# Performance work log

Measured on AMD Instinct MI355X. Metric: run time of the kernel, lower is better.

Reference implementation:

```python
import jax, jax.numpy as jnp
import numpy as np

SEQ = 4096
STATE_DIM = 512
ACTION_DIM = 496
T_DIM = 16
EMBED = STATE_DIM + ACTION_DIM + T_DIM  # 1024
HEADS = 4
HEAD_DIM = EMBED // HEADS
FF = 4096
N_EXP = 8
TOP_K = 2
EPS = 1e-5


def _ln(x, g, b):
    m = jnp.mean(x, -1, keepdims=True)
    v = jnp.var(x, -1, keepdims=True)
    return (x - m) * jax.lax.rsqrt(v + EPS) * g + b


def setup_inputs() -> dict:
    key = jax.random.key(0)
    ks = jax.random.split(key, 24)
    s = lambda k, shape, scale=0.02: jax.random.normal(k, shape, dtype=jnp.float32) * scale
    return {
        "x": jax.random.normal(ks[0], (SEQ, ACTION_DIM), dtype=jnp.float32),
        "time": jax.random.randint(ks[1], (SEQ,), 0, 6),
        "state": jax.random.normal(ks[2], (SEQ, 1, STATE_DIM), dtype=jnp.float32),
        "time_table": s(ks[3], (6, T_DIM), 1.0),
        "expert_w": s(ks[4], (N_EXP, EMBED, EMBED)),   # [n, in, out]
        "expert_b": jnp.zeros((N_EXP, EMBED), jnp.float32),
        "gate_w": s(ks[5], (EMBED, N_EXP)),
        "gate_b": jnp.zeros((N_EXP,), jnp.float32),
        "in_proj_w": s(ks[6], (EMBED, 3 * EMBED)),
        "in_proj_b": jnp.zeros((3 * EMBED,), jnp.float32),
        "out_proj_w": s(ks[7], (EMBED, EMBED)),
        "out_proj_b": jnp.zeros((EMBED,), jnp.float32),
        "ln1_g": jnp.ones((EMBED,), jnp.float32),
        "ln1_b": jnp.zeros((EMBED,), jnp.float32),
        "ff1_w": s(ks[8], (EMBED, FF)),
        "ff1_b": jnp.zeros((FF,), jnp.float32),
        "ff2_w": s(ks[9], (FF, ACTION_DIM)),
        "ff2_b": jnp.zeros((ACTION_DIM,), jnp.float32),
        "ln2_g": jnp.ones((ACTION_DIM,), jnp.float32),
        "ln2_b": jnp.zeros((ACTION_DIM,), jnp.float32),
    }


def reference(x, time, state, time_table, expert_w, expert_b, gate_w, gate_b,
              in_proj_w, in_proj_b, out_proj_w, out_proj_b,
              ln1_g, ln1_b, ff1_w, ff1_b, ff2_w, ff2_b, ln2_g, ln2_b):
    # combine inputs -> [S, EMBED]
    t_emb = time_table[time]                      # [S, t_dim]
    h = jnp.concatenate([x, t_emb, state[:, 0, :]], axis=-1)

    # MoE: softmax gate, top-k combine over densely-computed expert outputs
    gate = jax.nn.softmax(h @ gate_w + gate_b, axis=-1)      # [S, N]
    scores, idx = jax.lax.top_k(gate, TOP_K)                 # [S, K]
    all_out = jnp.einsum('se,nef->snf', h, expert_w) + expert_b[None]  # [S, N, E]
    comb = jnp.zeros_like(gate).at[jnp.arange(SEQ)[:, None], idx].add(scores)
    moe = jnp.einsum('sn,snf->sf', comb, all_out)            # [S, E]

    # multi-head self-attention (torch nn.MultiheadAttention, unbatched)
    qkv = moe @ in_proj_w + in_proj_b
    q, k, v = jnp.split(qkv, 3, axis=-1)
    q = q.reshape(SEQ, HEADS, HEAD_DIM) * (HEAD_DIM ** -0.5)
    k = k.reshape(SEQ, HEADS, HEAD_DIM)
    v = v.reshape(SEQ, HEADS, HEAD_DIM)
    att = jax.nn.softmax(jnp.einsum('shd,thd->hst', q, k), axis=-1)
    ao = jnp.einsum('hst,thd->shd', att, v).reshape(SEQ, EMBED)
    ao = ao @ out_proj_w + out_proj_b

    out1 = _ln(moe + ao, ln1_g, ln1_b)
    ff = jax.nn.relu(out1 @ ff1_w + ff1_b) @ ff2_w + ff2_b   # [S, action_dim]
    return _ln(ff, ln2_g, ln2_b)
```

## Files before the change

kernel.cpp:

```cpp
#include <hip/hip_runtime.h>
#include <hip/hip_bf16.h>
#include <hip/hip_fp8.h>

typedef __hip_bfloat16 hb;
typedef __bf16 bf16x8 __attribute__((ext_vector_type(8)));
typedef float f32x4 __attribute__((ext_vector_type(4)));

#define SEQ 4096
#define EMBED 1024
#define NHEAD 4
#define HDIM 256
#define FFD 4096
#define NEXP 8
#define ADIM 496
#define NSLOT 9216

static __device__ __forceinline__ float b2f(hb x) { return __bfloat162float(x); }
static __device__ __forceinline__ hb f2b(float x) { return __float2bfloat16(x); }
static __device__ __forceinline__ unsigned char f2e4m3(float v) {
  __hip_fp8_e4m3 t(v);
  return t.__x;
}
static __device__ __forceinline__ unsigned char f2e4m3_fast(float x) {
  unsigned u = __float_as_uint(x);
  u += 0x7FFFFu + ((u >> 20) & 1u);
  return (unsigned char)((u >> 20) - 960u);
}

#define GLOAD_LDS16(g, l)                                                      \
  __builtin_amdgcn_global_load_lds(                                            \
      (const __attribute__((address_space(1))) void*)(g),                      \
      (__attribute__((address_space(3))) void*)(l), 16, 0, 0)

#define GEMM_KLOOP64(KMAX)                                                     \
  for (int kt = 0; kt < (KMAX); kt += 64) {                                    \
    GLOAD_LDS16(Ag + kt, sA + wave * 512);                                     \
    GLOAD_LDS16(Ag + kt + 32, sA + 4096 + wave * 512);                         \
    GLOAD_LDS16(Ag + kt + 64 * lda_, sA + 2048 + wave * 512);                  \
    GLOAD_LDS16(Ag + kt + 64 * lda_ + 32, sA + 6144 + wave * 512);             \
    GLOAD_LDS16(Bg + kt, sB + wave * 512);                                     \
    GLOAD_LDS16(Bg + kt + 32, sB + 4096 + wave * 512);                         \
    GLOAD_LDS16(Bg + kt + 64 * ldb_, sB + 2048 + wave * 512);                  \
    GLOAD_LDS16(Bg + kt + 64 * ldb_ + 32, sB + 6144 + wave * 512);             \
    __syncthreads();                                                           \
    _Pragma("unroll") for (int ks = 0; ks < 2; ks++) {                         \
      bf16x8 av[4], bv[4];                                                     \
      _Pragma("unroll") for (int i = 0; i < 4; i++) {                          \
        const int row = wr * 64 + i * 16 + lm;                                 \
        av[i] = *(const bf16x8*)&sA[ks * 4096 + row * 32 + sw8];               \
      }                                                                        \
      _Pragma("unroll") for (int i = 0; i < 4; i++) {                          \
        const int row = wc * 64 + i * 16 + lm;                                 \
        bv[i] = *(const bf16x8*)&sB[ks * 4096 + row * 32 + sw8];               \
      }                                                                        \
      _Pragma("unroll") for (int i = 0; i < 4; i++)                            \
          _Pragma("unroll") for (int j = 0; j < 4; j++) acc[i][j] =            \
          __builtin_amdgcn_mfma_f32_16x16x32_bf16(av[i], bv[j], acc[i][j], 0,  \
                                                  0, 0);                       \
    }                                                                          \
    __syncthreads();                                                           \
  }

#define GEMM_PROLOGUE                                                          \
  const int m0 = blockIdx.y * 128, n0 = blockIdx.x * 128;                      \
  const int tid = threadIdx.x;                                                 \
  const int wave = tid >> 6, lane = tid & 63;                                  \
  const int quad = lane >> 4, lm = lane & 15;                                  \
  const int wr = wave >> 1, wc = wave & 1;                                     \
  const int r0 = tid >> 2;                                                     \
  const int cg = 8 * ((tid & 3) ^ ((tid >> 2) & 3));                           \
  const int sw8 = (quad ^ (lm & 3)) * 8;

#define EPILOGUE_B16(DST, LDC)                                                 \
  {                                                                            \
    hb* eb = smem + wave * 1024;                                               \
    _Pragma("unroll") for (int i = 0; i < 4; i++) {                            \
      _Pragma("unroll") for (int j = 0; j < 4; j++) {                          \
        const int c = ((j ^ quad) << 4) + lm;                                  \
        _Pragma("unroll") for (int rr = 0; rr < 4; rr++)                       \
            eb[(quad * 4 + rr) * 64 + c] = f2b(acc[i][j][rr]);                 \
      }                                                                        \
      _Pragma("unroll") for (int p = 0; p < 2; p++) {                          \
        const int r = p * 8 + (lane >> 3);                                     \
        const int cgc = lane & 7;                                              \
        const int gs = (cgc >> 1) ^ (r >> 2);                                  \
        const bf16x8 val =                                                     \
            *(const bf16x8*)&eb[r * 64 + gs * 16 + (cgc & 1) * 8];             \
        const long grow = m0 + wr * 64 + i * 16 + r;                           \
        *(bf16x8*)&DST[grow * (LDC) + n0 + wc * 64 + cgc * 8] = val;           \
      }                                                                        \
    }                                                                          \
  }

__global__ __launch_bounds__(256) void gemm_bt(
    const hb* __restrict__ A, long lda, long bA,
    const hb* __restrict__ B, long ldb, long bB,
    hb* __restrict__ C, long ldc, long bC,
    int K, const float* __restrict__ bias, int relu) {
  __shared__ __align__(16) hb smem[2 * 128 * 64];
  hb* sA = smem;
  hb* sB = smem + 8192;
  const int z = blockIdx.z;
  A += (long)z * bA;
  B += (long)z * bB;
  C += (long)z * bC;
  GEMM_PROLOGUE
  const long lda_ = lda, ldb_ = ldb;
  const hb* Ag = A + (long)(m0 + r0) * lda + cg;
  const hb* Bg = B + (long)(n0 + r0) * ldb + cg;

  f32x4 acc[4][4] = {};
  GEMM_KLOOP64(K)

  hb* eb = smem + wave * 1024;
#pragma unroll
  for (int i = 0; i < 4; i++) {
#pragma unroll
    for (int j = 0; j < 4; j++) {
      const float bval = bias ? bias[n0 + wc * 64 + j * 16 + lm] : 0.f;
      const int c = ((j ^ quad) << 4) + lm;
#pragma unroll
      for (int rr = 0; rr < 4; rr++) {
        float v = acc[i][j][rr] + bval;
        if (relu) v = fmaxf(v, 0.f);
        eb[(quad * 4 + rr) * 64 + c] = f2b(v);
      }
    }
#pragma unroll
    for (int p = 0; p < 2; p++) {
      const int r = p * 8 + (lane >> 3);
      const int cgc = lane & 7;
      const int gs = (cgc >> 1) ^ (r >> 2);
      const bf16x8 val = *(const bf16x8*)&eb[r * 64 + gs * 16 + (cgc & 1) * 8];
      const long grow = m0 + wr * 64 + i * 16 + r;
      *(bf16x8*)&C[grow * ldc + n0 + wc * 64 + cgc * 8] = val;
    }
  }
}

__global__ __launch_bounds__(256) void gemm_bt_exp(
    const hb* __restrict__ A, long lda, long bA,
    const hb* __restrict__ B, long ldb, long bB,
    unsigned char* __restrict__ C, long ldc, long bC,
    int K, float scale, hb* __restrict__ rsP) {
  __shared__ __align__(16) hb smem[2 * 128 * 64];
  hb* sA = smem;
  hb* sB = smem + 8192;
  const int z = blockIdx.z;
  A += (long)z * bA;
  B += (long)z * bB;
  C += (long)z * bC;
  GEMM_PROLOGUE
  const long lda_ = lda, ldb_ = ldb;
  const hb* Ag = A + (long)(m0 + r0) * lda + cg;
  const hb* Bg = B + (long)(n0 + r0) * ldb + cg;

  f32x4 acc[4][4] = {};
  GEMM_KLOOP64(K)

  unsigned char* eb8 = (unsigned char*)smem + wave * 1024;
  float* rbuf = (float*)sB;
  float rs[4][4];
#pragma unroll
  for (int i = 0; i < 4; i++) {
    float r4[4] = {0.f, 0.f, 0.f, 0.f};
#pragma unroll
    for (int j = 0; j < 4; j++) {
      const int c = ((j ^ quad) << 4) + lm;
#pragma unroll
      for (int rr = 0; rr < 4; rr++) {
        const float e =
            fminf(fmaxf(__expf(acc[i][j][rr] * scale), 0.015625f), 448.f);
        r4[rr] += e;
        eb8[(quad * 4 + rr) * 64 + c] = f2e4m3_fast(e);
      }
    }
#pragma unroll
    for (int rr = 0; rr < 4; rr++) {
      r4[rr] += __shfl_xor(r4[rr], 1);
      r4[rr] += __shfl_xor(r4[rr], 2);
      r4[rr] += __shfl_xor(r4[rr], 4);
      r4[rr] += __shfl_xor(r4[rr], 8);
      rs[i][rr] = r4[rr];
    }
    {
      const int r = lane >> 2;
      const int cgc = lane & 3;
      const f32x4 val =
          *(const f32x4*)&eb8[r * 64 + ((cgc ^ (r >> 2)) << 4)];
      const long grow = m0 + wr * 64 + i * 16 + r;
      *(f32x4*)&C[grow * ldc + n0 + wc * 64 + cgc * 16] = val;
    }
  }
  if (lm == 0) {
#pragma unroll
    for (int i = 0; i < 4; i++)
#pragma unroll
      for (int rr = 0; rr < 4; rr++)
        rbuf[(wr * 2 + wc) * 64 + i * 16 + quad * 4 + rr] = rs[i][rr];
  }
  __syncthreads();
  if (tid < 128) {
    const int lwr = tid >> 6, r64 = tid & 63;
    const float d = rbuf[lwr * 128 + r64] + rbuf[lwr * 128 + 64 + r64];
    rsP[((long)blockIdx.x * gridDim.z + z) * SEQ + m0 + lwr * 64 + r64] =
        f2b(d);
  }
}

__global__ __launch_bounds__(256) void pv_f8_splitk(
    const unsigned char* __restrict__ S, const unsigned char* __restrict__ Vt,
    hb* __restrict__ Cp) {
  const int z = blockIdx.z;
  const int head = z >> 1, split = z & 1;
  const unsigned char* A = S + (long)head * SEQ * SEQ + split * 2048;
  const unsigned char* B = Vt + ((long)head << 20) + split * 2048;
  hb* Cb = Cp + (long)z * SEQ * 256;
  __shared__ __align__(16) unsigned char smem8[16384];
  hb* smem = (hb*)smem8;
  unsigned char* sA8 = smem8;
  unsigned char* sB8 = smem8 + 8192;
  const int m0 = blockIdx.y * 128, n0 = blockIdx.x * 128;
  const int tid = threadIdx.x;
  const int wave = tid >> 6, lane = tid & 63;
  const int quad = lane >> 4, lm = lane & 15;
  const int wr = wave >> 1, wc = wave & 1;
  const int r8 = tid >> 2;
  const int cg8 = 16 * ((tid & 3) ^ (r8 & 3));
  const unsigned char* Ag = A + (long)(m0 + r8) * 4096 + cg8;
  const unsigned char* Bg = B + (long)(n0 + r8) * 4096 + cg8;

  f32x4 acc[4][4] = {};
  for (int kt = 0; kt < 2048; kt += 64) {
    GLOAD_LDS16(Ag + kt, sA8 + wave * 1024);
    GLOAD_LDS16(Ag + kt + 64 * 4096, sA8 + 4096 + wave * 1024);
    GLOAD_LDS16(Bg + kt, sB8 + wave * 1024);
    GLOAD_LDS16(Bg + kt + 64 * 4096, sB8 + 4096 + wave * 1024);
    __syncthreads();
#pragma unroll
    for (int ks = 0; ks < 2; ks++) {
      long a8[4], b8[4];
#pragma unroll
      for (int i = 0; i < 4; i++) {
        const int row = wr * 64 + i * 16 + lm;
        a8[i] = *(const long*)&sA8[row * 64 +
                                   (((ks * 2 + (quad >> 1)) ^ (row & 3)) << 4) +
                                   (quad & 1) * 8];
      }
#pragma unroll
      for (int i = 0; i < 4; i++) {
        const int row = wc * 64 + i * 16 + lm;
        b8[i] = *(const long*)&sB8[row * 64 +
                                   (((ks * 2 + (quad >> 1)) ^ (row & 3)) << 4) +
                                   (quad & 1) * 8];
      }
#pragma unroll
      for (int i = 0; i < 4; i++)
#pragma unroll
        for (int j = 0; j < 4; j++)
          acc[i][j] = __builtin_amdgcn_mfma_f32_16x16x32_fp8_fp8(
              a8[i], b8[j], acc[i][j], 0, 0, 0);
    }
    __syncthreads();
  }
  EPILOGUE_B16(Cb, 256)
}

__global__ __launch_bounds__(256) void gemm_bt_splitk(
    const hb* __restrict__ A, long lda, long bA,
    const hb* __restrict__ B, long ldb, long bB,
    float* __restrict__ Cp, int ldcp, long pstride, int Ksub, int shift) {
  const int z = blockIdx.z;
  const int batch = z >> shift, split = z - (batch << shift);
  A += (long)batch * bA + (long)split * Ksub;
  B += (long)batch * bB + (long)split * Ksub;
  Cp += (long)z * pstride;
  __shared__ __align__(16) hb smem[2 * 128 * 64];
  hb* sA = smem;
  hb* sB = smem + 8192;
  GEMM_PROLOGUE
  const long lda_ = lda, ldb_ = ldb;
  const hb* Ag = A + (long)(m0 + r0) * lda + cg;
  const hb* Bg = B + (long)(n0 + r0) * ldb + cg;

  f32x4 acc[4][4] = {};
  GEMM_KLOOP64(Ksub)

  float* ef = (float*)smem + wave * 1024;
#pragma unroll
  for (int i = 0; i < 4; i++) {
#pragma unroll
    for (int j = 0; j < 4; j++) {
      const int c = ((j ^ quad) << 4) + lm;
#pragma unroll
      for (int rr = 0; rr < 4; rr++)
        ef[(quad * 4 + rr) * 64 + c] = acc[i][j][rr];
    }
#pragma unroll
    for (int p = 0; p < 4; p++) {
      const int r = p * 4 + (lane >> 4);
      const int cgc = lane & 15;
      const int gs = (cgc >> 2) ^ (r >> 2);
      const f32x4 val = *(const f32x4*)&ef[r * 64 + gs * 16 + (cgc & 3) * 4];
      const long grow = m0 + wr * 64 + i * 16 + r;
      *(f32x4*)&Cp[grow * ldcp + n0 + wc * 64 + cgc * 4] = val;
    }
  }
}

__global__ __launch_bounds__(256) void gemm_bt_splitk_b16(
    const hb* __restrict__ A, long lda, long bA,
    const hb* __restrict__ B, long ldb, long bB,
    hb* __restrict__ Cp, int ldcp, long pstride, int Ksub, int shift) {
  const int z = blockIdx.z;
  const int batch = z >> shift, split = z - (batch << shift);
  A += (long)batch * bA + (long)split * Ksub;
  B += (long)batch * bB + (long)split * Ksub;
  Cp += (long)z * pstride;
  __shared__ __align__(16) hb smem[2 * 128 * 64];
  hb* sA = smem;
  hb* sB = smem + 8192;
  GEMM_PROLOGUE
  const long lda_ = lda, ldb_ = ldb;
  const hb* Ag = A + (long)(m0 + r0) * lda + cg;
  const hb* Bg = B + (long)(n0 + r0) * ldb + cg;

  f32x4 acc[4][4] = {};
  GEMM_KLOOP64(Ksub)
  EPILOGUE_B16(Cp, ldcp)
}

__global__ __launch_bounds__(256) void reduce_splitk(
    const float* __restrict__ part, long pstride, int nsplit, int shift,
    hb* __restrict__ C, long ldc, long bC, int Nshift) {
  const long idx = (long)blockIdx.x * 256 + threadIdx.x;
  const int batch = blockIdx.y;
  float v = 0.f;
  for (int k = 0; k < nsplit; k++)
    v += part[(long)((batch << shift) + k) * pstride + idx];
  const long row = idx >> Nshift;
  const long col = idx & ((1 << Nshift) - 1);
  C[(long)batch * bC + row * ldc + col] = f2b(v);
}

__global__ __launch_bounds__(256) void reduce_pv(
    const hb* __restrict__ part, const hb* __restrict__ rsP,
    hb* __restrict__ ao) {
  const int row = blockIdx.x, head = blockIdx.y, tid = threadIdx.x;
  __shared__ float dsh;
  if (tid < 64) {
    float p = b2f(rsP[((long)(tid & 31) * NHEAD + head) * SEQ + row]);
#pragma unroll
    for (int o = 32; o; o >>= 1) p += __shfl_down(p, o);
    if (tid == 0) dsh = 0.5f * p;
  }
  __syncthreads();
  const float den = dsh;
  const long base = ((long)(head * 2) * SEQ + row) * 256 + tid;
  const float v = b2f(part[base]) + b2f(part[base + (long)SEQ * 256]);
  ao[(long)row * 1024 + head * 256 + tid] = f2b(v / den);
}

__global__ __launch_bounds__(256) void gemm_moe(
    const hb* __restrict__ h, const hb* __restrict__ expertT,
    const int* __restrict__ slot_token, const int* __restrict__ eblk,
    hb* __restrict__ slotout) {
  const int e = eblk[blockIdx.y];
  if (e < 0) return;
  __shared__ __align__(16) hb smem[2 * 128 * 64];
  hb* sA = smem;
  hb* sB = smem + 8192;
  GEMM_PROLOGUE
  const int t0 = slot_token[m0 + r0];
  const int t1 = slot_token[m0 + r0 + 64];
  const hb* B = expertT + ((long)e << 20);
  const hb* Ag0 = h + (long)t0 * EMBED + cg;
  const hb* Ag1 = h + (long)t1 * EMBED + cg;
  const hb* Bg = B + (long)(n0 + r0) * EMBED + cg;

  f32x4 acc[4][4] = {};
  for (int kt = 0; kt < EMBED; kt += 64) {
    GLOAD_LDS16(Ag0 + kt, sA + wave * 512);
    GLOAD_LDS16(Ag0 + kt + 32, sA + 4096 + wave * 512);
    GLOAD_LDS16(Ag1 + kt, sA + 2048 + wave * 512);
    GLOAD_LDS16(Ag1 + kt + 32, sA + 6144 + wave * 512);
    GLOAD_LDS16(Bg + kt, sB + wave * 512);
    GLOAD_LDS16(Bg + kt + 32, sB + 4096 + wave * 512);
    GLOAD_LDS16(Bg + kt + 64 * EMBED, sB + 2048 + wave * 512);
    GLOAD_LDS16(Bg + kt + 64 * EMBED + 32, sB + 6144 + wave * 512);
    __syncthreads();
#pragma unroll
    for (int ks = 0; ks < 2; ks++) {
      bf16x8 av[4], bv[4];
#pragma unroll
      for (int i = 0; i < 4; i++) {
        const int row = wr * 64 + i * 16 + lm;
        av[i] = *(const bf16x8*)&sA[ks * 4096 + row * 32 + sw8];
      }
#pragma unroll
      for (int i = 0; i < 4; i++) {
        const int row = wc * 64 + i * 16 + lm;
        bv[i] = *(const bf16x8*)&sB[ks * 4096 + row * 32 + sw8];
      }
#pragma unroll
      for (int i = 0; i < 4; i++)
#pragma unroll
        for (int j = 0; j < 4; j++)
          acc[i][j] = __builtin_amdgcn_mfma_f32_16x16x32_bf16(av[i], bv[j],
                                                              acc[i][j], 0, 0, 0);
    }
    __syncthreads();
  }
  EPILOGUE_B16(slotout, EMBED)
}

__global__ __launch_bounds__(256) void transpose_all(
    const float* __restrict__ expert_w, const float* __restrict__ in_proj_w,
    const float* __restrict__ out_proj_w, const float* __restrict__ ff1_w,
    const float* __restrict__ ff2_w, hb* __restrict__ expertT,
    hb* __restrict__ inprojT, hb* __restrict__ outprojT, hb* __restrict__ ff1T,
    hb* __restrict__ ff2T) {
  const int b = blockIdx.x;
  const float* in;
  hb* outp;
  int R, Cin, Cout, ldin, ldout, bx, by;
  if (b < 8192) {
    const int z = b >> 10, l = b & 1023;
    bx = l & 31; by = l >> 5;
    in = expert_w + (long)z * 1048576; outp = expertT + (long)z * 1048576;
    R = 1024; Cin = 1024; Cout = 1024; ldin = 1024; ldout = 1024;
  } else if (b < 11264) {
    const int l = b - 8192;
    bx = l % 96; by = l / 96;
    in = in_proj_w; outp = inprojT;
    R = 1024; Cin = 3072; Cout = 3072; ldin = 3072; ldout = 1024;
  } else if (b < 12288) {
    const int l = b - 11264;
    bx = l & 31; by = l >> 5;
    in = out_proj_w; outp = outprojT;
    R = 1024; Cin = 1024; Cout = 1024; ldin = 1024; ldout = 1024;
  } else if (b < 16384) {
    const int l = b - 12288;
    bx = l & 127; by = l >> 7;
    in = ff1_w; outp = ff1T;
    R = 1024; Cin = 4096; Cout = 4096; ldin = 4096; ldout = 1024;
  } else {
    const int l = b - 16384;
    bx = l & 15; by = l >> 4;
    in = ff2_w; outp = ff2T;
    R = 4096; Cin = 496; Cout = 512; ldin = 496; ldout = 4096;
  }
  __shared__ hb tile[32][33];
  const int c0 = bx * 32, r0 = by * 32;
  const int tx = threadIdx.x, ty = threadIdx.y;
#pragma unroll
  for (int i = 0; i < 32; i += 8) {
    const int r = r0 + ty + i, c = c0 + tx;
    hb v = f2b(0.f);
    if (r < R && c < Cin) v = f2b(in[(long)r * ldin + c]);
    tile[ty + i][tx] = v;
  }
  __syncthreads();
#pragma unroll
  for (int i = 0; i < 32; i += 8) {
    const int c = c0 + ty + i, r = r0 + tx;
    if (c < Cout && r < R) outp[(long)c * ldout + r] = tile[tx][ty + i];
  }
}

__global__ __launch_bounds__(256) void transpose_v(
    const hb* __restrict__ in, hb* __restrict__ out) {
  __shared__ hb tile[32][33];
  const int z = blockIdx.z;
  in += (long)z * 256;
  out += (long)z * 1048576;
  const int c0 = blockIdx.x * 32, r0 = blockIdx.y * 32;
  const int tx = threadIdx.x, ty = threadIdx.y;
#pragma unroll
  for (int i = 0; i < 32; i += 8)
    tile[ty + i][tx] = in[(long)(r0 + ty + i) * 3072 + c0 + tx];
  __syncthreads();
#pragma unroll
  for (int i = 0; i < 32; i += 8)
    out[(long)(c0 + ty + i) * 4096 + r0 + tx] = tile[tx][ty + i];
}

__global__ __launch_bounds__(256) void transpose_v8(
    const hb* __restrict__ in, unsigned char* __restrict__ out) {
  __shared__ hb tile[32][33];
  const int z = blockIdx.z;
  in += (long)z * 256;
  out += (long)z * 1048576;
  const int c0 = blockIdx.x * 32, r0 = blockIdx.y * 32;
  const int tx = threadIdx.x, ty = threadIdx.y;
#pragma unroll
  for (int i = 0; i < 32; i += 8)
    tile[ty + i][tx] = in[(long)(r0 + ty + i) * 3072 + c0 + tx];
  __syncthreads();
#pragma unroll
  for (int i = 0; i < 32; i += 8)
    out[(long)(c0 + ty + i) * 4096 + r0 + tx] = f2e4m3(b2f(tile[tx][ty + i]));
}

__global__ __launch_bounds__(256) void bh_gate_kernel(
    const float* __restrict__ x, const int* __restrict__ timev,
    const float* __restrict__ state, const float* __restrict__ ttab,
    const float* __restrict__ gw, const float* __restrict__ gb,
    hb* __restrict__ h, int* __restrict__ tok_e, float* __restrict__ tok_w) {
  const int s = blockIdx.x, tid = threadIdx.x;
  const int wv = tid >> 6, ln = tid & 63;
  const int t = timev[s];
  float acc[8] = {0, 0, 0, 0, 0, 0, 0, 0};
  for (int c = tid; c < EMBED; c += 256) {
    float v;
    if (c < ADIM)
      v = x[(long)s * ADIM + c];
    else if (c < ADIM + 16)
      v = ttab[t * 16 + (c - ADIM)];
    else
      v = state[(long)s * 512 + (c - 512)];
    h[(long)s * EMBED + c] = f2b(v);
    const float* g = gw + c * 8;
#pragma unroll
    for (int n = 0; n < 8; n++) acc[n] += v * g[n];
  }
#pragma unroll
  for (int o = 32; o; o >>= 1)
#pragma unroll
    for (int n = 0; n < 8; n++) acc[n] += __shfl_down(acc[n], o);
  __shared__ float red[4][8];
  if (ln == 0)
#pragma unroll
    for (int n = 0; n < 8; n++) red[wv][n] = acc[n];
  __syncthreads();
  if (tid == 0) {
    float lg[8], m = -1e30f;
    for (int n = 0; n < 8; n++) {
      lg[n] = red[0][n] + red[1][n] + red[2][n] + red[3][n] + gb[n];
      m = fmaxf(m, lg[n]);
    }
    float den = 0.f;
    for (int n = 0; n < 8; n++) {
      lg[n] = expf(lg[n] - m);
      den += lg[n];
    }
    for (int n = 0; n < 8; n++) lg[n] /= den;
    int i1 = 0;
    for (int n = 1; n < 8; n++)
      if (lg[n] > lg[i1]) i1 = n;
    int i2 = (i1 == 0) ? 1 : 0;
    for (int n = 0; n < 8; n++) {
      if (n == i1) continue;
      if (lg[n] > lg[i2]) i2 = n;
    }
    tok_e[2 * s] = i1;
    tok_w[2 * s] = lg[i1];
    tok_e[2 * s + 1] = i2;
    tok_w[2 * s + 1] = lg[i2];
  }
}

__global__ __launch_bounds__(256) void group_kernel(
    const int* __restrict__ tok_e, int* __restrict__ slot_token,
    int* __restrict__ token_slot, int* __restrict__ eblk) {
  __shared__ int cnt[8], off[9], cur[8];
  const int tid = threadIdx.x;
  if (tid < 8) cnt[tid] = 0;
  for (int i = tid; i < NSLOT; i += 256) slot_token[i] = 0;
  __syncthreads();
  for (int i = tid; i < 2 * SEQ; i += 256) atomicAdd(&cnt[tok_e[i]], 1);
  __syncthreads();
  if (tid == 0) {
    int o = 0;
    for (int n = 0; n < 8; n++) {
      off[n] = o;
      cur[n] = o;
      o += (cnt[n] + 127) & ~127;
    }
    off[8] = o;
  }
  __syncthreads();
  if (tid < NSLOT / 128) {
    const int rb = tid * 128;
    int e = -1;
    for (int n = 0; n < 8; n++)
      if (rb >= off[n] && rb < off[n + 1]) e = n;
    eblk[tid] = e;
  }
  for (int i = tid; i < 2 * SEQ; i += 256) {
    const int e = tok_e[i];
    const int slot = atomicAdd(&cur[e], 1);
    slot_token[slot] = i >> 1;
    token_slot[i] = slot;
  }
}

__global__ __launch_bounds__(256) void moe_combine_kernel(
    const hb* __restrict__ slotout, const int* __restrict__ token_slot,
    const float* __restrict__ tok_w, const int* __restrict__ tok_e,
    const float* __restrict__ eb, hb* __restrict__ moe) {
  const int s = blockIdx.x, tid = threadIdx.x;
  const int s0 = token_slot[2 * s], s1 = token_slot[2 * s + 1];
  const float w0 = tok_w[2 * s], w1 = tok_w[2 * s + 1];
  const int e0 = tok_e[2 * s], e1 = tok_e[2 * s + 1];
  const hb* r0 = slotout + (long)s0 * EMBED;
  const hb* r1 = slotout + (long)s1 * EMBED;
  const float* b0 = eb + e0 * EMBED;
  const float* b1 = eb + e1 * EMBED;
  for (int c = tid; c < EMBED; c += 256) {
    const float v = w0 * (b2f(r0[c]) + b0[c]) + w1 * (b2f(r1[c]) + b1[c]);
    moe[(long)s * EMBED + c] = f2b(v);
  }
}

__global__ __launch_bounds__(256) void softmax_fast(hb* __restrict__ S,
                                                    float scale) {
  const long row = blockIdx.x;
  const int tid = threadIdx.x, wv = tid >> 6, ln = tid & 63;
  hb* p = S + row * 4096 + tid * 16;
  __shared__ float red[4];
  bf16x8 a0 = *(const bf16x8*)p;
  bf16x8 a1 = *(const bf16x8*)(p + 8);
  float v[16];
#pragma unroll
  for (int i = 0; i < 8; i++) {
    v[i] = (float)a0[i];
    v[8 + i] = (float)a1[i];
  }
  float m = v[0];
#pragma unroll
  for (int i = 1; i < 16; i++) m = fmaxf(m, v[i]);
#pragma unroll
  for (int o = 32; o; o >>= 1) m = fmaxf(m, __shfl_down(m, o));
  if (ln == 0) red[wv] = m;
  __syncthreads();
  const float M = fmaxf(fmaxf(red[0], red[1]), fmaxf(red[2], red[3])) * scale;
  __syncthreads();
  float sum = 0.f;
#pragma unroll
  for (int i = 0; i < 16; i++) {
    v[i] = __expf(v[i] * scale - M);
    sum += v[i];
  }
#pragma unroll
  for (int o = 32; o; o >>= 1) sum += __shfl_down(sum, o);
  if (ln == 0) red[wv] = sum;
  __syncthreads();
  const float inv = 1.f / (red[0] + red[1] + red[2] + red[3]);
#pragma unroll
  for (int i = 0; i < 8; i++) {
    a0[i] = (__bf16)(v[i] * inv);
    a1[i] = (__bf16)(v[8 + i] * inv);
  }
  *(bf16x8*)p = a0;
  *(bf16x8*)(p + 8) = a1;
}

__global__ __launch_bounds__(256) void ln_kernel(
    const hb* __restrict__ in, long ldin, const hb* __restrict__ resid,
    long ldr, const float* __restrict__ g, const float* __restrict__ beta,
    hb* __restrict__ outb, long ldout, int ncol) {
  const int s = blockIdx.x, tid = threadIdx.x, wv = tid >> 6, ln = tid & 63;
  __shared__ float buf[1024];
  __shared__ float red[4];
  float sum = 0.f, sq = 0.f;
  for (int c = tid; c < ncol; c += 256) {
    float v = b2f(in[(long)s * ldin + c]);
    if (resid) v += b2f(resid[(long)s * ldr + c]);
    buf[c] = v;
    sum += v;
    sq += v * v;
  }
#pragma unroll
  for (int o = 32; o; o >>= 1) sum += __shfl_down(sum, o);
  if (ln == 0) red[wv] = sum;
  __syncthreads();
  const float S = red[0] + red[1] + red[2] + red[3];
  __syncthreads();
#pragma unroll
  for (int o = 32; o; o >>= 1) sq += __shfl_down(sq, o);
  if (ln == 0) red[wv] = sq;
  __syncthreads();
  const float Q = red[0] + red[1] + red[2] + red[3];
  const float mean = S / ncol;
  const float var = Q / ncol - mean * mean;
  const float r = rsqrtf(var + 1e-5f);
  for (int c = tid; c < ncol; c += 256)
    outb[(long)s * ldout + c] = f2b((buf[c] - mean) * r * g[c] + beta[c]);
}

__global__ __launch_bounds__(256) void ln2_red_kernel(
    const float* __restrict__ part, long pstride,
    const float* __restrict__ bias, const float* __restrict__ g,
    const float* __restrict__ beta, float* __restrict__ out) {
  const int s = blockIdx.x, tid = threadIdx.x, wv = tid >> 6, ln = tid & 63;
  __shared__ float buf[512];
  __shared__ float red[4];
  float sum = 0.f, sq = 0.f;
  for (int c = tid; c < ADIM; c += 256) {
    const long idx = (long)s * 512 + c;
    float v = part[idx] + part[pstride + idx] + part[2 * pstride + idx] +
              part[3 * pstride + idx] + bias[c];
    buf[c] = v;
    sum += v;
    sq += v * v;
  }
#pragma unroll
  for (int o = 32; o; o >>= 1) sum += __shfl_down(sum, o);
  if (ln == 0) red[wv] = sum;
  __syncthreads();
  const float S = red[0] + red[1] + red[2] + red[3];
  __syncthreads();
#pragma unroll
  for (int o = 32; o; o >>= 1) sq += __shfl_down(sq, o);
  if (ln == 0) red[wv] = sq;
  __syncthreads();
  const float Q = red[0] + red[1] + red[2] + red[3];
  const float mean = S / ADIM;
  const float var = Q / ADIM - mean * mean;
  const float r = rsqrtf(var + 1e-5f);
  for (int c = tid; c < ADIM; c += 256)
    out[(long)s * ADIM + c] = (buf[c] - mean) * r * g[c] + beta[c];
}

__global__ __launch_bounds__(256) void ln2_red_b16_kernel(
    const hb* __restrict__ part, long pstride,
    const float* __restrict__ bias, const float* __restrict__ g,
    const float* __restrict__ beta, float* __restrict__ out) {
  const int s = blockIdx.x, tid = threadIdx.x, wv = tid >> 6, ln = tid & 63;
  __shared__ float buf[512];
  __shared__ float red[4];
  float sum = 0.f, sq = 0.f;
  for (int c = tid; c < ADIM; c += 256) {
    const long idx = (long)s * 512 + c;
    float v = b2f(part[idx]) + b2f(part[pstride + idx]) +
              b2f(part[2 * pstride + idx]) + b2f(part[3 * pstride + idx]) +
              bias[c];
    buf[c] = v;
    sum += v;
    sq += v * v;
  }
#pragma unroll
  for (int o = 32; o; o >>= 1) sum += __shfl_down(sum, o);
  if (ln == 0) red[wv] = sum;
  __syncthreads();
  const float S = red[0] + red[1] + red[2] + red[3];
  __syncthreads();
#pragma unroll
  for (int o = 32; o; o >>= 1) sq += __shfl_down(sq, o);
  if (ln == 0) red[wv] = sq;
  __syncthreads();
  const float Q = red[0] + red[1] + red[2] + red[3];
  const float mean = S / ADIM;
  const float var = Q / ADIM - mean * mean;
  const float r = rsqrtf(var + 1e-5f);
  for (int c = tid; c < ADIM; c += 256)
    out[(long)s * ADIM + c] = (buf[c] - mean) * r * g[c] + beta[c];
}

extern "C" void kernel_launch(void* const* d_in, const int* in_sizes, int n_in,
                              void* d_out, int out_size, void* d_ws,
                              size_t ws_size, hipStream_t stream) {
  const float* x = (const float*)d_in[0];
  const int* timev = (const int*)d_in[1];
  const float* state = (const float*)d_in[2];
  const float* ttab = (const float*)d_in[3];
  const float* expert_w = (const float*)d_in[4];
  const float* expert_b = (const float*)d_in[5];
  const float* gate_w = (const float*)d_in[6];
  const float* gate_b = (const float*)d_in[7];
  const float* in_proj_w = (const float*)d_in[8];
  const float* in_proj_b = (const float*)d_in[9];
  const float* out_proj_w = (const float*)d_in[10];
  const float* out_proj_b = (const float*)d_in[11];
  const float* ln1_g = (const float*)d_in[12];
  const float* ln1_b = (const float*)d_in[13];
  const float* ff1_w = (const float*)d_in[14];
  const float* ff1_b = (const float*)d_in[15];
  const float* ff2_w = (const float*)d_in[16];
  const float* ff2_b = (const float*)d_in[17];
  const float* ln2_g = (const float*)d_in[18];
  const float* ln2_b = (const float*)d_in[19];
  float* out = (float*)d_out;

  char* w = (char*)d_ws;
  const long MB = 1048576;
  const bool big = ws_size >= (size_t)(192 * MB);

  hb* expertT = (hb*)(w + 0 * MB);
  hb* slotout = (hb*)(w + 16 * MB);
  hb* h = (hb*)(w + 35 * MB);
  hb* inprojT = (hb*)(w + 43 * MB);
  hb* outprojT = (hb*)(w + (big ? 168 : 49) * MB);
  hb* ff1T = (hb*)(w + (big ? 170 : 51) * MB);
  hb* ff2T = (hb*)(w + (big ? 178 : 59) * MB);
  const long metaOff = (big ? 190 : 63) * MB;
  int* tok_e = (int*)(w + metaOff);
  float* tok_w = (float*)(w + metaOff + 32768);
  int* slot_token = (int*)(w + metaOff + 65536);
  int* token_slot = (int*)(w + metaOff + 102400);
  int* eblk = (int*)(w + metaOff + 135168);
  hb* rsP = (hb*)(w + metaOff + 163840);
  hb* moe = (hb*)(w + (big ? 152 : 64) * MB);
  hb* qkv = (hb*)(w + (big ? 0 : 72) * MB);
  unsigned char* scores8 = (unsigned char*)(w + 24 * MB);
  hb* scores = (hb*)(w + 96 * MB);
  unsigned char* vt8 = (unsigned char*)(w + 160 * MB);
  hb* vt = (hb*)(w + 8 * MB);
  hb* ao = (hb*)(w + (big ? 182 : 0) * MB);
  hb* ao2 = (hb*)(w + (big ? 24 : 8) * MB);
  hb* out1 = (hb*)(w + (big ? 32 : 132) * MB);
  hb* ffmid = (hb*)(w + (big ? 40 : 96) * MB);
  float* part = (float*)(w + (big ? 72 : 16) * MB);
  hb* partb16 = (hb*)(w + (big ? 72 : 16) * MB);
  hb* pvpart = (hb*)(w + 0 * MB);
  (void)in_sizes; (void)n_in; (void)out_size;

  transpose_all<<<dim3(18432), dim3(32, 8), 0, stream>>>(
      expert_w, in_proj_w, out_proj_w, ff1_w, ff2_w, expertT, inprojT, outprojT,
      ff1T, ff2T);

  bh_gate_kernel<<<dim3(SEQ), 256, 0, stream>>>(x, timev, state, ttab, gate_w,
                                                gate_b, h, tok_e, tok_w);
  group_kernel<<<dim3(1), 256, 0, stream>>>(tok_e, slot_token, token_slot, eblk);

  gemm_moe<<<dim3(8, NSLOT / 128), 256, 0, stream>>>(h, expertT, slot_token,
                                                     eblk, slotout);
  moe_combine_kernel<<<dim3(SEQ), 256, 0, stream>>>(slotout, token_slot, tok_w,
                                                    tok_e, expert_b, moe);

  gemm_bt<<<dim3(24, 32, 1), 256, 0, stream>>>(moe, 1024, 0, inprojT, 1024, 0,
                                               qkv, 3072, 0, 1024, in_proj_b, 0);
  if (big)
    transpose_v8<<<dim3(8, 128, 4), dim3(32, 8), 0, stream>>>(qkv + 2048, vt8);
  else
    transpose_v<<<dim3(8, 128, 4), dim3(32, 8), 0, stream>>>(qkv + 2048, vt);

  if (big) {
    gemm_bt_exp<<<dim3(32, 32, 4), 256, 0, stream>>>(
        qkv, 3072, 256, qkv + 1024, 3072, 256, scores8, 4096, (long)SEQ * SEQ,
        HDIM, 0.0625f, rsP);
    pv_f8_splitk<<<dim3(2, 32, 8), 256, 0, stream>>>(scores8, vt8, pvpart);
    reduce_pv<<<dim3(4096, 4), 256, 0, stream>>>(pvpart, rsP, ao);
  } else {
    for (int hp = 0; hp < 2; ++hp) {
      const hb* qb = qkv + hp * 512;
      const hb* kb = qkv + 1024 + hp * 512;
      gemm_bt<<<dim3(32, 32, 2), 256, 0, stream>>>(
          qb, 3072, 256, kb, 3072, 256, scores, 4096, (long)SEQ * SEQ, HDIM,
          nullptr, 0);
      softmax_fast<<<dim3(2 * SEQ), 256, 0, stream>>>(scores, 0.0625f);
      gemm_bt_splitk<<<dim3(2, 32, 8), 256, 0, stream>>>(
          scores, 4096, (long)SEQ * SEQ, vt + (long)hp * 2097152, 4096,
          1048576L, part, 256, (long)SEQ * 256, 1024, 2);
      reduce_splitk<<<dim3(4096, 2), 256, 0, stream>>>(
          part, (long)SEQ * 256, 4, 2, ao + hp * 512, 1024, 256, 8);
    }
  }

  gemm_bt<<<dim3(8, 32, 1), 256, 0, stream>>>(ao, 1024, 0, outprojT, 1024, 0,
                                              ao2, 1024, 0, 1024, out_proj_b, 0);
  ln_kernel<<<dim3(SEQ), 256, 0, stream>>>(moe, 1024, ao2, 1024, ln1_g, ln1_b,
                                           out1, 1024, 1024);

  gemm_bt<<<dim3(32, 32, 1), 256, 0, stream>>>(out1, 1024, 0, ff1T, 1024, 0,
                                               ffmid, 4096, 0, 1024, ff1_b, 1);
  if (big) {
    gemm_bt_splitk_b16<<<dim3(4, 32, 4), 256, 0, stream>>>(
        ffmid, 4096, 0, ff2T, 4096, 0, partb16, 512, (long)SEQ * 512, 1024, 2);
    ln2_red_b16_kernel<<<dim3(SEQ), 256, 0, stream>>>(
        partb16, (long)SEQ * 512, ff2_b, ln2_g, ln2_b, out);
  } else {
    gemm_bt_splitk<<<dim3(4, 32, 4), 256, 0, stream>>>(
        ffmid, 4096, 0, ff2T, 4096, 0, part, 512, (long)SEQ * 512, 1024, 2);
    ln2_red_kernel<<<dim3(SEQ), 256, 0, stream>>>(part, (long)SEQ * 512, ff2_b,
                                                  ln2_g, ln2_b, out);
  }
}
```

Measured before the change: 522.1 us.

## Vectorize weight transpose and elementwise kernels with wide loads and stores

Rewrites the fp32-to-bf16 weight transpose to use 64-row tiles, float4 reads, a swizzled shared tile and 16-byte bf16 stores, which halves the block count. The gate/concat, MoE combine, LayerNorm and PV-reduce kernels move from per-element accesses to 4-wide vector loads and stores. reduce_pv now handles four rows per block, and the duplicate lane sum is dropped from its denominator. The aim is to cut memory-transaction overhead in these bandwidth-bound kernels. The cost is tighter alignment and divisibility assumptions on the data shapes.

```diff
diff --git a/kernel.cpp b/kernel.cpp
--- a/kernel.cpp
+++ b/kernel.cpp
@@ -4,6 +4,7 @@
 
 typedef __hip_bfloat16 hb;
 typedef __bf16 bf16x8 __attribute__((ext_vector_type(8)));
+typedef __bf16 bf16x4 __attribute__((ext_vector_type(4)));
 typedef float f32x4 __attribute__((ext_vector_type(4)));
 
 #define SEQ 4096
@@ -346,19 +347,26 @@
 __global__ __launch_bounds__(256) void reduce_pv(
     const hb* __restrict__ part, const hb* __restrict__ rsP,
     hb* __restrict__ ao) {
-  const int row = blockIdx.x, head = blockIdx.y, tid = threadIdx.x;
-  __shared__ float dsh;
-  if (tid < 64) {
-    float p = b2f(rsP[((long)(tid & 31) * NHEAD + head) * SEQ + row]);
-#pragma unroll
-    for (int o = 32; o; o >>= 1) p += __shfl_down(p, o);
-    if (tid == 0) dsh = 0.5f * p;
-  }
-  __syncthreads();
-  const float den = dsh;
-  const long base = ((long)(head * 2) * SEQ + row) * 256 + tid;
-  const float v = b2f(part[base]) + b2f(part[base + (long)SEQ * 256]);
-  ao[(long)row * 1024 + head * 256 + tid] = f2b(v / den);
+  const int rb = blockIdx.x * 4, head = blockIdx.y, tid = threadIdx.x;
+  __shared__ float dsh[4];
+  if (tid < 128) {
+    const int r = tid >> 5, nb = tid & 31;
+    float p = b2f(rsP[((long)nb * NHEAD + head) * SEQ + rb + r]);
+#pragma unroll
+    for (int o = 16; o; o >>= 1) p += __shfl_down(p, o, 32);
+    if (nb == 0) dsh[r] = p;
+  }
+  __syncthreads();
+  const int r = tid >> 6, c4 = (tid & 63) * 4;
+  const float den = dsh[r];
+  const long base = ((long)(head * 2) * SEQ + rb + r) * 256 + c4;
+  const bf16x4 p0 = *(const bf16x4*)&part[base];
+  const bf16x4 p1 = *(const bf16x4*)&part[base + (long)SEQ * 256];
+  bf16x4 o4;
+#pragma unroll
+  for (int k = 0; k < 4; k++)
+    o4[k] = (__bf16)(((float)p0[k] + (float)p1[k]) / den);
+  *(bf16x4*)&ao[(long)(rb + r) * 1024 + head * 256 + c4] = o4;
 }
 
 __global__ __launch_bounds__(256) void gemm_moe(
@@ -423,48 +431,57 @@
   const int b = blockIdx.x;
   const float* in;
   hb* outp;
-  int R, Cin, Cout, ldin, ldout, bx, by;
-  if (b < 8192) {
-    const int z = b >> 10, l = b & 1023;
+  int Cin, ldin, ldout, bx, by;
+  if (b < 4096) {
+    const int z = b >> 9, l = b & 511;
     bx = l & 31; by = l >> 5;
     in = expert_w + (long)z * 1048576; outp = expertT + (long)z * 1048576;
-    R = 1024; Cin = 1024; Cout = 1024; ldin = 1024; ldout = 1024;
-  } else if (b < 11264) {
-    const int l = b - 8192;
+    Cin = 1024; ldin = 1024; ldout = 1024;
+  } else if (b < 5632) {
+    const int l = b - 4096;
     bx = l % 96; by = l / 96;
     in = in_proj_w; outp = inprojT;
-    R = 1024; Cin = 3072; Cout = 3072; ldin = 3072; ldout = 1024;
-  } else if (b < 12288) {
-    const int l = b - 11264;
+    Cin = 3072; ldin = 3072; ldout = 1024;
+  } else if (b < 6144) {
+    const int l = b - 5632;
     bx = l & 31; by = l >> 5;
     in = out_proj_w; outp = outprojT;
-    R = 1024; Cin = 1024; Cout = 1024; ldin = 1024; ldout = 1024;
-  } else if (b < 16384) {
-    const int l = b - 12288;
+    Cin = 1024; ldin = 1024; ldout = 1024;
+  } else if (b < 8192) {
+    const int l = b - 6144;
     bx = l & 127; by = l >> 7;
     in = ff1_w; outp = ff1T;
-    R = 1024; Cin = 4096; Cout = 4096; ldin = 4096; ldout = 1024;
+    Cin = 4096; ldin = 4096; ldout = 1024;
   } else {
-    const int l = b - 16384;
+    const int l = b - 8192;
     bx = l & 15; by = l >> 4;
     in = ff2_w; outp = ff2T;
-    R = 4096; Cin = 496; Cout = 512; ldin = 496; ldout = 4096;
-  }
-  __shared__ hb tile[32][33];
-  const int c0 = bx * 32, r0 = by * 32;
-  const int tx = threadIdx.x, ty = threadIdx.y;
-#pragma unroll
-  for (int i = 0; i < 32; i += 8) {
-    const int r = r0 + ty + i, c = c0 + tx;
-    hb v = f2b(0.f);
-    if (r < R && c < Cin) v = f2b(in[(long)r * ldin + c]);
-    tile[ty + i][tx] = v;
-  }
-  __syncthreads();
-#pragma unroll
-  for (int i = 0; i < 32; i += 8) {
-    const int c = c0 + ty + i, r = r0 + tx;
-    if (c < Cout && r < R) outp[(long)c * ldout + r] = tile[tx][ty + i];
+    Cin = 496; ldin = 496; ldout = 4096;
+  }
+  __shared__ hb tile[32][72];
+  const int c0 = bx * 32, r0 = by * 64;
+  const int t = threadIdx.x;
+  {
+    const int rr = t >> 2, cb = (t & 3) * 8;
+    const int c = c0 + cb;
+    float v[8] = {0, 0, 0, 0, 0, 0, 0, 0};
+    if (c < Cin) {
+      const f32x4 p0 = *(const f32x4*)&in[(long)(r0 + rr) * ldin + c];
+      const f32x4 p1 = *(const f32x4*)&in[(long)(r0 + rr) * ldin + c + 4];
+#pragma unroll
+      for (int k = 0; k < 4; k++) { v[k] = p0[k]; v[4 + k] = p1[k]; }
+    }
+#pragma unroll
+    for (int j = 0; j < 8; j++) {
+      const int cidx = cb + j;
+      tile[cidx][rr ^ ((((cidx) >> 3) & 3) << 3)] = f2b(v[j]);
+    }
+  }
+  __syncthreads();
+  {
+    const int oc = t >> 3, seg = t & 7;
+    const bf16x8 val = *(const bf16x8*)&tile[oc][(seg ^ ((oc >> 3) & 3)) * 8];
+    *(bf16x8*)&outp[(long)(c0 + oc) * ldout + r0 + seg * 8] = val;
   }
 }
 
@@ -510,19 +527,24 @@
   const int s = blockIdx.x, tid = threadIdx.x;
   const int wv = tid >> 6, ln = tid & 63;
   const int t = timev[s];
+  const int c = tid * 4;
+  f32x4 v4;
+  if (c < ADIM)
+    v4 = *(const f32x4*)&x[(long)s * ADIM + c];
+  else if (c < 512)
+    v4 = *(const f32x4*)&ttab[t * 16 + (c - ADIM)];
+  else
+    v4 = *(const f32x4*)&state[(long)s * 512 + (c - 512)];
+  bf16x4 h4;
+#pragma unroll
+  for (int k = 0; k < 4; k++) h4[k] = (__bf16)v4[k];
+  *(bf16x4*)&h[(long)s * EMBED + c] = h4;
   float acc[8] = {0, 0, 0, 0, 0, 0, 0, 0};
-  for (int c = tid; c < EMBED; c += 256) {
-    float v;
-    if (c < ADIM)
-      v = x[(long)s * ADIM + c];
-    else if (c < ADIM + 16)
-      v = ttab[t * 16 + (c - ADIM)];
-    else
-      v = state[(long)s * 512 + (c - 512)];
-    h[(long)s * EMBED + c] = f2b(v);
-    const float* g = gw + c * 8;
-#pragma unroll
-    for (int n = 0; n < 8; n++) acc[n] += v * g[n];
+#pragma unroll
+  for (int k = 0; k < 4; k++) {
+    const float* g = gw + (c + k) * 8;
+#pragma unroll
+    for (int n = 0; n < 8; n++) acc[n] += v4[k] * g[n];
   }
 #pragma unroll
   for (int o = 32; o; o >>= 1)
@@ -603,14 +625,16 @@
   const int s0 = token_slot[2 * s], s1 = token_slot[2 * s + 1];
   const float w0 = tok_w[2 * s], w1 = tok_w[2 * s + 1];
   const int e0 = tok_e[2 * s], e1 = tok_e[2 * s + 1];
-  const hb* r0 = slotout + (long)s0 * EMBED;
-  const hb* r1 = slotout + (long)s1 * EMBED;
-  const float* b0 = eb + e0 * EMBED;
-  const float* b1 = eb + e1 * EMBED;
-  for (int c = tid; c < EMBED; c += 256) {
-    const float v = w0 * (b2f(r0[c]) + b0[c]) + w1 * (b2f(r1[c]) + b1[c]);
-    moe[(long)s * EMBED + c] = f2b(v);
-  }
+  const int c = tid * 4;
+  const bf16x4 a0 = *(const bf16x4*)&slotout[(long)s0 * EMBED + c];
+  const bf16x4 a1 = *(const bf16x4*)&slotout[(long)s1 * EMBED + c];
+  const f32x4 b0 = *(const f32x4*)&eb[e0 * EMBED + c];
+  const f32x4 b1 = *(const f32x4*)&eb[e1 * EMBED + c];
+  bf16x4 o4;
+#pragma unroll
+  for (int k = 0; k < 4; k++)
+    o4[k] = (__bf16)(w0 * ((float)a0[k] + b0[k]) + w1 * ((float)a1[k] + b1[k]));
+  *(bf16x4*)&moe[(long)s * EMBED + c] = o4;
 }
 
 __global__ __launch_bounds__(256) void softmax_fast(hb* __restrict__ S,
@@ -664,12 +688,24 @@
   __shared__ float buf[1024];
   __shared__ float red[4];
   float sum = 0.f, sq = 0.f;
-  for (int c = tid; c < ncol; c += 256) {
-    float v = b2f(in[(long)s * ldin + c]);
-    if (resid) v += b2f(resid[(long)s * ldr + c]);
-    buf[c] = v;
-    sum += v;
-    sq += v * v;
+  for (int c = tid * 4; c < ncol; c += 1024) {
+    const bf16x4 iv = *(const bf16x4*)&in[(long)s * ldin + c];
+#pragma unroll
+    for (int k = 0; k < 4; k++) {
+      float v = (float)iv[k];
+      buf[c + k] = v;
+    }
+    if (resid) {
+      const bf16x4 rv = *(const bf16x4*)&resid[(long)s * ldr + c];
+#pragma unroll
+      for (int k = 0; k < 4; k++) buf[c + k] += (float)rv[k];
+    }
+#pragma unroll
+    for (int k = 0; k < 4; k++) {
+      const float v = buf[c + k];
+      sum += v;
+      sq += v * v;
+    }
   }
 #pragma unroll
   for (int o = 32; o; o >>= 1) sum += __shfl_down(sum, o);
@@ -685,8 +721,15 @@
   const float mean = S / ncol;
   const float var = Q / ncol - mean * mean;
   const float r = rsqrtf(var + 1e-5f);
-  for (int c = tid; c < ncol; c += 256)
-    outb[(long)s * ldout + c] = f2b((buf[c] - mean) * r * g[c] + beta[c]);
+  for (int c = tid * 4; c < ncol; c += 1024) {
+    const f32x4 gv = *(const f32x4*)&g[c];
+    const f32x4 bv = *(const f32x4*)&beta[c];
+    bf16x4 o4;
+#pragma unroll
+    for (int k = 0; k < 4; k++)
+      o4[k] = (__bf16)((buf[c + k] - mean) * r * gv[k] + bv[k]);
+    *(bf16x4*)&outb[(long)s * ldout + c] = o4;
+  }
 }
 
 __global__ __launch_bounds__(256) void ln2_red_kernel(
@@ -731,14 +774,22 @@
   __shared__ float buf[512];
   __shared__ float red[4];
   float sum = 0.f, sq = 0.f;
-  for (int c = tid; c < ADIM; c += 256) {
+  const int c = tid * 4;
+  if (c < ADIM) {
     const long idx = (long)s * 512 + c;
-    float v = b2f(part[idx]) + b2f(part[pstride + idx]) +
-              b2f(part[2 * pstride + idx]) + b2f(part[3 * pstride + idx]) +
-              bias[c];
-    buf[c] = v;
-    sum += v;
-    sq += v * v;
+    const bf16x4 p0 = *(const bf16x4*)&part[idx];
+    const bf16x4 p1 = *(const bf16x4*)&part[pstride + idx];
+    const bf16x4 p2 = *(const bf16x4*)&part[2 * pstride + idx];
+    const bf16x4 p3 = *(const bf16x4*)&part[3 * pstride + idx];
+    const f32x4 bv = *(const f32x4*)&bias[c];
+#pragma unroll
+    for (int k = 0; k < 4; k++) {
+      const float v = (float)p0[k] + (float)p1[k] + (float)p2[k] +
+                      (float)p3[k] + bv[k];
+      buf[c + k] = v;
+      sum += v;
+      sq += v * v;
+    }
   }
 #pragma unroll
   for (int o = 32; o; o >>= 1) sum += __shfl_down(sum, o);
@@ -754,8 +805,15 @@
   const float mean = S / ADIM;
   const float var = Q / ADIM - mean * mean;
   const float r = rsqrtf(var + 1e-5f);
-  for (int c = tid; c < ADIM; c += 256)
-    out[(long)s * ADIM + c] = (buf[c] - mean) * r * g[c] + beta[c];
+  if (c < ADIM) {
+    const f32x4 gv = *(const f32x4*)&g[c];
+    const f32x4 bt = *(const f32x4*)&beta[c];
+    f32x4 o4;
+#pragma unroll
+    for (int k = 0; k < 4; k++)
+      o4[k] = (buf[c + k] - mean) * r * gv[k] + bt[k];
+    *(f32x4*)&out[(long)s * ADIM + c] = o4;
+  }
 }
 
 extern "C" void kernel_launch(void* const* d_in, const int* in_sizes, int n_in,
@@ -816,7 +874,7 @@
   hb* pvpart = (hb*)(w + 0 * MB);
   (void)in_sizes; (void)n_in; (void)out_size;
 
-  transpose_all<<<dim3(18432), dim3(32, 8), 0, stream>>>(
+  transpose_all<<<dim3(9216), dim3(256), 0, stream>>>(
       expert_w, in_proj_w, out_proj_w, ff1_w, ff2_w, expertT, inprojT, outprojT,
       ff1T, ff2T);
 
@@ -841,7 +899,7 @@
         qkv, 3072, 256, qkv + 1024, 3072, 256, scores8, 4096, (long)SEQ * SEQ,
         HDIM, 0.0625f, rsP);
     pv_f8_splitk<<<dim3(2, 32, 8), 256, 0, stream>>>(scores8, vt8, pvpart);
-    reduce_pv<<<dim3(4096, 4), 256, 0, stream>>>(pvpart, rsP, ao);
+    reduce_pv<<<dim3(1024, 4), 256, 0, stream>>>(pvpart, rsP, ao);
   } else {
     for (int hp = 0; hp < 2; ++hp) {
       const hb* qb = qkv + hp * 512;
```

New measurement: 514.7 us. Within noise of the previous version (-1.4%).
